# Optimization experiments

Hardware: AMD Instinct MI355X
Metric: run time of the kernel (lower is better)

Reference implementation:

```python
import jax, jax.numpy as jnp
import numpy as np


def _gru(x, h0, Wi, Wh, bi, bh):
    """PyTorch-equations GRU. x: (T,B,D), Wi: (3H,D), Wh: (3H,H). Returns (ys, hT)."""
    xW = jnp.einsum('tbd,gd->tbg', x, Wi) + bi  # (T,B,3H) precomputed input proj
    def step(h, xw):
        hw = h @ Wh.T + bh
        xr, xz, xn = jnp.split(xw, 3, axis=-1)
        hr, hz, hn = jnp.split(hw, 3, axis=-1)
        r = jax.nn.sigmoid(xr + hr)
        z = jax.nn.sigmoid(xz + hz)
        n = jnp.tanh(xn + r * hn)
        h_new = (1.0 - z) * n + z * h
        return h_new, h_new
    hT, ys = jax.lax.scan(step, h0, xW)
    return ys, hT


def _bigru(x, WiF, WhF, biF, bhF, WiB, WhB, biB, bhB):
    B = x.shape[1]
    H = WhF.shape[1]
    h0 = jnp.zeros((B, H), x.dtype)
    yf, hf = _gru(x, h0, WiF, WhF, biF, bhF)
    yb, hb = _gru(x[::-1], h0, WiB, WhB, biB, bhB)
    return jnp.concatenate([yf, yb[::-1]], axis=-1), jnp.stack([hf, hb], axis=0)


def _ln(x, g, b, eps=1e-5):
    mu = x.mean(-1, keepdims=True)
    var = ((x - mu) ** 2).mean(-1, keepdims=True)
    return (x - mu) * jax.lax.rsqrt(var + eps) * g + b


def _forward(tokens, emb,
             s_WiF, s_WhF, s_biF, s_bhF, s_lnF_g, s_lnF_b,
             s_Wi_f, s_Wh_f, s_bi_f, s_bh_f, s_Wi_b, s_Wh_b, s_bi_b, s_bh_b,
             s_ln_g, s_ln_b, s_linW, s_linb,
             d_WiF, d_WhF, d_biF, d_bhF, d_lnF_g, d_lnF_b,
             d_Wi_f, d_Wh_f, d_bi_f, d_bh_f, d_Wi_b, d_Wh_b, d_bi_b, d_bh_b,
             d_ln_g, d_ln_b, out_W, out_b):
    S, T, B = tokens.shape
    H = s_WhF.shape[1]
    # sentence loop is batch-independent -> fold sentences into batch
    x = emb[tokens]                                  # (S,T,B,E)
    x = x.transpose(1, 0, 2, 3).reshape(T, S * B, -1)  # (T, S*B, E)
    h0 = jnp.zeros((S * B, H), x.dtype)
    y, _ = _gru(x, h0, s_WiF, s_WhF, s_biF, s_bhF)
    y = _ln(y, s_lnF_g, s_lnF_b)
    y, _ = _bigru(y, s_Wi_f, s_Wh_f, s_bi_f, s_bh_f, s_Wi_b, s_Wh_b, s_bi_b, s_bh_b)
    y = _ln(y, s_ln_g, s_ln_b)
    y = jnp.tanh(y @ s_linW.T + s_linb)              # (T, S*B, H)
    store = y.mean(axis=0).reshape(S, B, H)          # per-sentence mean-pooled cell
    # document-level encoder over sentence sequence
    h0d = jnp.zeros((B, H), x.dtype)
    y, _ = _gru(store, h0d, d_WiF, d_WhF, d_biF, d_bhF)
    y = _ln(y, d_lnF_g, d_lnF_b)
    y, _ = _bigru(y, d_Wi_f, d_Wh_f, d_bi_f, d_bh_f, d_Wi_b, d_Wh_b, d_bi_b, d_bh_b)
    y = _ln(y, d_ln_g, d_ln_b)
    return jax.nn.sigmoid(y @ out_W.T + out_b)       # (S, B, O)


def setup_inputs() -> dict:
    V, E, H, O = 32000, 256, 256, 2
    S, T, B = 96, 32, 32
    keys = iter(jax.random.split(jax.random.key(0), 64))
    def g(shape, scale=0.06):
        return jax.random.normal(next(keys), shape, jnp.float32) * scale
    inp = {}
    inp['tokens'] = jax.random.randint(next(keys), (S, T, B), 0, V)
    inp['emb'] = g((V, E), 0.1)
    # sentence encoder: uni GRU (E->H), LN(H), bi GRU (H->H), LN(2H), linear 2H->H
    inp['s_WiF'] = g((3 * H, E)); inp['s_WhF'] = g((3 * H, H))
    inp['s_biF'] = jnp.zeros((3 * H,)); inp['s_bhF'] = jnp.zeros((3 * H,))
    inp['s_lnF_g'] = jnp.ones((H,)); inp['s_lnF_b'] = jnp.zeros((H,))
    inp['s_Wi_f'] = g((3 * H, H)); inp['s_Wh_f'] = g((3 * H, H))
    inp['s_bi_f'] = jnp.zeros((3 * H,)); inp['s_bh_f'] = jnp.zeros((3 * H,))
    inp['s_Wi_b'] = g((3 * H, H)); inp['s_Wh_b'] = g((3 * H, H))
    inp['s_bi_b'] = jnp.zeros((3 * H,)); inp['s_bh_b'] = jnp.zeros((3 * H,))
    inp['s_ln_g'] = jnp.ones((2 * H,)); inp['s_ln_b'] = jnp.zeros((2 * H,))
    inp['s_linW'] = g((H, 2 * H)); inp['s_linb'] = jnp.zeros((H,))
    # document encoder: uni GRU (H->H), LN(H), bi GRU (H->H), LN(2H)
    inp['d_WiF'] = g((3 * H, H)); inp['d_WhF'] = g((3 * H, H))
    inp['d_biF'] = jnp.zeros((3 * H,)); inp['d_bhF'] = jnp.zeros((3 * H,))
    inp['d_lnF_g'] = jnp.ones((H,)); inp['d_lnF_b'] = jnp.zeros((H,))
    inp['d_Wi_f'] = g((3 * H, H)); inp['d_Wh_f'] = g((3 * H, H))
    inp['d_bi_f'] = jnp.zeros((3 * H,)); inp['d_bh_f'] = jnp.zeros((3 * H,))
    inp['d_Wi_b'] = g((3 * H, H)); inp['d_Wh_b'] = g((3 * H, H))
    inp['d_bi_b'] = jnp.zeros((3 * H,)); inp['d_bh_b'] = jnp.zeros((3 * H,))
    inp['d_ln_g'] = jnp.ones((2 * H,)); inp['d_ln_b'] = jnp.zeros((2 * H,))
    inp['out_W'] = g((O, 2 * H)); inp['out_b'] = jnp.zeros((O,))
    return inp


def reference(tokens, emb,
              s_WiF, s_WhF, s_biF, s_bhF, s_lnF_g, s_lnF_b,
              s_Wi_f, s_Wh_f, s_bi_f, s_bh_f, s_Wi_b, s_Wh_b, s_bi_b, s_bh_b,
              s_ln_g, s_ln_b, s_linW, s_linb,
              d_WiF, d_WhF, d_biF, d_bhF, d_lnF_g, d_lnF_b,
              d_Wi_f, d_Wh_f, d_bi_f, d_bh_f, d_Wi_b, d_Wh_b, d_bi_b, d_bh_b,
              d_ln_g, d_ln_b, out_W, out_b):
    return _forward(tokens, emb,
                    s_WiF, s_WhF, s_biF, s_bhF, s_lnF_g, s_lnF_b,
                    s_Wi_f, s_Wh_f, s_bi_f, s_bh_f, s_Wi_b, s_Wh_b, s_bi_b, s_bh_b,
                    s_ln_g, s_ln_b, s_linW, s_linb,
                    d_WiF, d_WhF, d_biF, d_bhF, d_lnF_g, d_lnF_b,
                    d_Wi_f, d_Wh_f, d_bi_f, d_bh_f, d_Wi_b, d_Wh_b, d_bi_b, d_bh_b,
                    d_ln_g, d_ln_b, out_W, out_b)
```

## Files before the change

kernel.cpp:

```cpp
#include <hip/hip_runtime.h>


typedef __bf16 bf16;
typedef __bf16 bf16x8 __attribute__((ext_vector_type(8)));
typedef __bf16 bf16x4 __attribute__((ext_vector_type(4)));
typedef float  f32x4  __attribute__((ext_vector_type(4)));

static __device__ __forceinline__ f32x4 mfma16(bf16x8 a, bf16x8 b, f32x4 c) {
  return __builtin_amdgcn_mfma_f32_16x16x32_bf16(a, b, c, 0, 0, 0);
}
static __device__ __forceinline__ float sigm(float x) { return 1.f / (1.f + __expf(-x)); }
static __device__ __forceinline__ bf16x8 asbf(f32x4 v) {
  union { f32x4 f; bf16x8 b; } u; u.f = v; return u.b;
}
static __device__ __forceinline__ void wg_barrier() {
  asm volatile("s_waitcnt lgkmcnt(0)" ::: "memory");
  __builtin_amdgcn_s_barrier();
  __builtin_amdgcn_sched_barrier(0);
}
static __device__ __forceinline__ void gload16(const bf16* g, bf16* l) {
  __builtin_amdgcn_global_load_lds(
      (const __attribute__((address_space(1))) void*)g,
      (__attribute__((address_space(3))) void*)l, 16, 0, 0);
}

__global__ __launch_bounds__(256) void cvt_bf16(
    const float* __restrict__ s, bf16* __restrict__ d, int n4)
{
  int i = blockIdx.x * 256 + threadIdx.x;
  if (i < n4) {
    float4 v = ((const float4*)s)[i];
    bf16x4 o;
    o[0] = (bf16)v.x; o[1] = (bf16)v.y; o[2] = (bf16)v.z; o[3] = (bf16)v.w;
    ((bf16x4*)d)[i] = o;
  }
}

__global__ __launch_bounds__(256) void conv13(
    const float* s0, const float* s1, const float* s2, const float* s3,
    const float* s4, const float* s5, const float* s6, const float* s7,
    const float* s8, const float* s9, const float* s10, const float* s11,
    const float* s12, bf16* __restrict__ dst)
{
  const float* srcs[13] = {s0,s1,s2,s3,s4,s5,s6,s7,s8,s9,s10,s11,s12};
  int m = blockIdx.y;
  int n4 = (m == 12) ? 32768 : 49152;
  int i = blockIdx.x * 256 + threadIdx.x;
  if (i >= n4) return;
  float4 v = ((const float4*)srcs[m])[i];
  bf16x4 o;
  o[0] = (bf16)v.x; o[1] = (bf16)v.y; o[2] = (bf16)v.z; o[3] = (bf16)v.w;
  ((bf16x4*)(dst + (size_t)m * 196608))[i] = o;
}

__global__ __launch_bounds__(256) void prep_bias(
    const float* b0i, const float* b0h, const float* b1i, const float* b1h,
    const float* b2i, const float* b2h, const float* b3i, const float* b3h,
    const float* b4i, const float* b4h, const float* b5i, const float* b5h,
    float* __restrict__ out)
{
  const float* bis[6] = {b0i,b1i,b2i,b3i,b4i,b5i};
  const float* bhs[6] = {b0h,b1h,b2h,b3h,b4h,b5h};
  int g = blockIdx.y;
  int i = blockIdx.x * 256 + threadIdx.x;
  if (i < 768)
    out[g * 768 + i] = bis[g][i] + (i < 512 ? bhs[g][i] : 0.f);
}

__global__ __launch_bounds__(256) void xw_gemm(
    const bf16* __restrict__ X,
    const bf16* __restrict__ W0, const float* __restrict__ b0, bf16* __restrict__ o0,
    const bf16* __restrict__ W1, const float* __restrict__ b1, bf16* __restrict__ o1)
{
  const bf16* W = blockIdx.y ? W1 : W0;
  const float* bias = blockIdx.y ? b1 : b0;
  bf16* out = blockIdx.y ? o1 : o0;
  int wave = (int)blockIdx.x * 4 + (threadIdx.x >> 6);
  int g64 = wave / 48, ct = wave - g64 * 48;
  int lane = threadIdx.x & 63;
  int r16 = lane & 15, g4 = lane >> 4;
  const bf16* wp = W + (size_t)(ct * 16 + r16) * 256;
  const bf16* xb = X + ((size_t)g64 * 64 + r16) * 256;
  f32x4 a0 = {0,0,0,0}, a1 = {0,0,0,0}, a2 = {0,0,0,0}, a3 = {0,0,0,0};
#pragma unroll
  for (int kk = 0; kk < 8; kk++) {
    int k0 = kk * 32 + g4 * 8;
    bf16x8 wf = *(const bf16x8*)(wp + k0);
    a0 = mfma16(*(const bf16x8*)(xb + k0), wf, a0);
    a1 = mfma16(*(const bf16x8*)(xb + 4096 + k0), wf, a1);
    a2 = mfma16(*(const bf16x8*)(xb + 8192 + k0), wf, a2);
    a3 = mfma16(*(const bf16x8*)(xb + 12288 + k0), wf, a3);
  }
  float bv = bias[ct * 16 + r16];
#pragma unroll
  for (int rt = 0; rt < 4; rt++) {
    f32x4 ac = rt == 0 ? a0 : rt == 1 ? a1 : rt == 2 ? a2 : a3;
#pragma unroll
    for (int j = 0; j < 4; j++)
      out[(size_t)(g64 * 64 + rt * 16 + g4 * 4 + j) * 768 + ct * 16 + r16] = (bf16)(ac[j] + bv);
  }
}

__global__ __launch_bounds__(256) void xw_gather_gemm(
    const int* __restrict__ tok, const bf16* __restrict__ embb,
    const bf16* __restrict__ W, const float* __restrict__ bias,
    bf16* __restrict__ out, int c)
{
  int t = blockIdx.y;
  int wave = (int)blockIdx.x * 4 + (threadIdx.x >> 6);
  int g64 = wave / 48, ct = wave - g64 * 48;
  int lane = threadIdx.x & 63;
  int r16 = lane & 15, g4 = lane >> 4;
  const bf16* wp = W + (size_t)(ct * 16 + r16) * 256;
  const bf16* ap[4];
#pragma unroll
  for (int rt = 0; rt < 4; rt++) {
    int n = g64 * 64 + rt * 16 + r16;
    int tk = tok[((n >> 5) << 10) + (t << 5) + (n & 31)];
    ap[rt] = embb + (size_t)tk * 256;
  }
  f32x4 a0 = {0,0,0,0}, a1 = {0,0,0,0}, a2 = {0,0,0,0}, a3 = {0,0,0,0};
#pragma unroll
  for (int kk = 0; kk < 8; kk++) {
    int k0 = kk * 32 + g4 * 8;
    bf16x8 wf = *(const bf16x8*)(wp + k0);
    a0 = mfma16(*(const bf16x8*)(ap[0] + k0), wf, a0);
    a1 = mfma16(*(const bf16x8*)(ap[1] + k0), wf, a1);
    a2 = mfma16(*(const bf16x8*)(ap[2] + k0), wf, a2);
    a3 = mfma16(*(const bf16x8*)(ap[3] + k0), wf, a3);
  }
  float bv = bias[ct * 16 + r16];
#pragma unroll
  for (int rt = 0; rt < 4; rt++) {
    f32x4 ac = rt == 0 ? a0 : rt == 1 ? a1 : rt == 2 ? a2 : a3;
#pragma unroll
    for (int j = 0; j < 4; j++)
      out[((size_t)t * c + g64 * 64 + rt * 16 + g4 * 4 + j) * 768 + ct * 16 + r16] = (bf16)(ac[j] + bv);
  }
}

__global__ __launch_bounds__(1024)
__attribute__((amdgpu_waves_per_eu(4, 4)))
void pgru(
    const bf16* __restrict__ xw0, const bf16* __restrict__ Wh0, const float* __restrict__ bh0,
    const bf16* __restrict__ xw1, const bf16* __restrict__ Wh1, const float* __restrict__ bh1,
    bf16* __restrict__ yout0, bf16* __restrict__ yout1, int ostride,
    const float* __restrict__ lng, const float* __restrict__ lnb,
    int steps, int Mtot, int rev0, int rev1)
{
  int dir = blockIdx.y;
  const bf16*  xw = dir ? xw1 : xw0;
  const bf16*  Wh = dir ? Wh1 : Wh0;
  const float* bh = dir ? bh1 : bh0;
  bf16* yout = dir ? yout1 : yout0;
  int rev = dir ? rev1 : rev0;

  __shared__ __align__(16) bf16 hbuf[16][264];
  __shared__ __align__(16) bf16 xbuf[2][16][3][16][16];

  int tid = threadIdx.x;
  int w = tid >> 6, lane = tid & 63, r16 = lane & 15, g4 = lane >> 4;
  int rowbase = (int)blockIdx.x * 16;
  int c0 = w * 16 + r16;

  for (int i2 = tid; i2 < 528; i2 += 1024) ((bf16x8*)hbuf)[i2] = (bf16x8){};

  f32x4 wr[8], wz[8], wn[8];
  {
    const bf16* W0 = Wh + (size_t)c0 * 256;
#pragma unroll
    for (int kk = 0; kk < 8; kk++) {
      int k0 = kk * 32 + g4 * 8;
      wr[kk] = *(const f32x4*)(W0 + k0);          asm volatile("" : "+v"(wr[kk]));
      wz[kk] = *(const f32x4*)(W0 + 65536 + k0);  asm volatile("" : "+v"(wz[kk]));
      wn[kk] = *(const f32x4*)(W0 + 131072 + k0); asm volatile("" : "+v"(wn[kk]));
    }
  }
  float bhn0 = bh[c0 + 512];

  int m_ = (lane & 31) >> 1;
  int k_ = (lane & 1) * 8;
  int gsel = (lane >> 5) * 256;
  auto stage = [&](int b, int st) {
    const bf16* s1 = xw + ((size_t)st * Mtot + rowbase + m_) * 768 + gsel + w * 16 + k_;
    gload16(s1,       &xbuf[b][w][0][0][0]);
    gload16(s1 + 256, &xbuf[b][w][1][0][0]);
  };
  stage(0, rev ? steps - 1 : 0);

  for (int i = 0; i < steps; i++) {
    int cur = i & 1;
    int st = rev ? steps - 1 - i : i;
    if (i + 1 < steps) {
      stage(cur ^ 1, rev ? steps - 2 - i : i + 1);
      asm volatile("s_waitcnt vmcnt(2)" ::: "memory");
    } else {
      asm volatile("s_waitcnt vmcnt(0)" ::: "memory");
    }
    __builtin_amdgcn_sched_barrier(0);
    wg_barrier();

    f32x4 a0 = {0,0,0,0}, a1 = {0,0,0,0}, a2 = {0,0,0,0};
#pragma unroll
    for (int kk = 0; kk < 8; kk++) {
      bf16x8 a = *(const bf16x8*)&hbuf[r16][kk * 32 + g4 * 8];
      a0 = mfma16(a, asbf(wr[kk]), a0);
      a1 = mfma16(a, asbf(wz[kk]), a1);
      a2 = mfma16(a, asbf(wn[kk]), a2);
    }
    float hn[4];
#pragma unroll
    for (int j = 0; j < 4; j++) {
      int m = g4 * 4 + j;
      float r = sigm((float)xbuf[cur][w][0][m][r16] + a0[j]);
      float z = sigm((float)xbuf[cur][w][1][m][r16] + a1[j]);
      float n = tanhf((float)xbuf[cur][w][2][m][r16] + r * (a2[j] + bhn0));
      hn[j] = (1.f - z) * n + z * (float)hbuf[m][c0];
    }
    wg_barrier();
#pragma unroll
    for (int j = 0; j < 4; j++)
      hbuf[g4 * 4 + j][c0] = (bf16)hn[j];
    if (!lng) {
#pragma unroll
      for (int j = 0; j < 4; j++) {
        size_t ro = ((size_t)st * Mtot + rowbase + g4 * 4 + j) * ostride;
        yout[ro + c0] = (bf16)hn[j];
      }
    } else {
      wg_barrier();
      bf16x4 v4 = *(const bf16x4*)&hbuf[w][lane * 4];
      float v[4]; float sm = 0.f, sq = 0.f;
#pragma unroll
      for (int j = 0; j < 4; j++) { v[j] = (float)v4[j]; sm += v[j]; sq += v[j] * v[j]; }
      for (int msk = 32; msk; msk >>= 1) { sm += __shfl_xor(sm, msk); sq += __shfl_xor(sq, msk); }
      float mu  = sm * (1.f / 256.f);
      float var = sq * (1.f / 256.f) - mu * mu;
      float inv = rsqrtf(fmaxf(var, 0.f) + 1e-5f);
      bf16x4 o;
#pragma unroll
      for (int j = 0; j < 4; j++)
        o[j] = (bf16)((v[j] - mu) * inv * lng[lane * 4 + j] + lnb[lane * 4 + j]);
      *(bf16x4*)&yout[((size_t)st * Mtot + rowbase + w) * ostride + lane * 4] = o;
    }
  }
}

__global__ __launch_bounds__(256) void sent_tail_part(
    const bf16* __restrict__ hf, const bf16* __restrict__ hb,
    const float* __restrict__ gam, const float* __restrict__ bet,
    const bf16* __restrict__ W, const float* __restrict__ bias,
    float* __restrict__ part, int c)
{
  int wave = threadIdx.x >> 6;
  int lane = threadIdx.x & 63;
  int r16 = lane & 15, g4 = lane >> 4;
  int r0 = (int)blockIdx.x << 4;
  int tg = blockIdx.y;
  size_t rowoff = (size_t)(r0 + r16) * 256;

  f32x4 ms0 = {0,0,0,0}, ms1 = {0,0,0,0}, ms2 = {0,0,0,0}, ms3 = {0,0,0,0};

  for (int tt = 0; tt < 4; tt++) {
    int t = tg * 4 + tt;
    const bf16* pf = hf + (size_t)t * c * 256 + rowoff;
    const bf16* pb = hb + (size_t)t * c * 256 + rowoff;
    bf16x8 xv[16];
    float s = 0.f, sq = 0.f;
#pragma unroll
    for (int kk = 0; kk < 16; kk++) {
      int k0 = kk * 32 + g4 * 8;
      xv[kk] = (kk < 8) ? *(const bf16x8*)(pf + k0) : *(const bf16x8*)(pb + k0 - 256);
#pragma unroll
      for (int j = 0; j < 8; j++) { float f = (float)xv[kk][j]; s += f; sq += f * f; }
    }
    s  += __shfl_xor(s, 16);  s  += __shfl_xor(s, 32);
    sq += __shfl_xor(sq, 16); sq += __shfl_xor(sq, 32);
    float mu  = s * (1.f / 512.f);
    float var = sq * (1.f / 512.f) - mu * mu;
    float inv = rsqrtf(fmaxf(var, 0.f) + 1e-5f);
#pragma unroll
    for (int kk = 0; kk < 16; kk++) {
      int k0 = kk * 32 + g4 * 8;
      float ga[8], be[8];
      *(float4*)(ga)     = *(const float4*)(gam + k0);
      *(float4*)(ga + 4) = *(const float4*)(gam + k0 + 4);
      *(float4*)(be)     = *(const float4*)(bet + k0);
      *(float4*)(be + 4) = *(const float4*)(bet + k0 + 4);
#pragma unroll
      for (int j = 0; j < 8; j++)
        xv[kk][j] = (bf16)(((float)xv[kk][j] - mu) * inv * ga[j] + be[j]);
    }
#pragma unroll
    for (int tc = 0; tc < 4; tc++) {
      int cj = wave * 64 + tc * 16;
      const bf16* wp = W + (size_t)(cj + r16) * 512;
      f32x4 acc = {0,0,0,0};
#pragma unroll
      for (int kk = 0; kk < 16; kk++)
        acc = mfma16(xv[kk], *(const bf16x8*)(wp + kk * 32 + g4 * 8), acc);
      float bb = bias[cj + r16];
      f32x4* msp = (tc == 0) ? &ms0 : (tc == 1) ? &ms1 : (tc == 2) ? &ms2 : &ms3;
#pragma unroll
      for (int j = 0; j < 4; j++) (*msp)[j] += tanhf(acc[j] + bb);
    }
  }
#pragma unroll
  for (int tc = 0; tc < 4; tc++) {
    int cj = wave * 64 + tc * 16;
    f32x4 ms = (tc == 0) ? ms0 : (tc == 1) ? ms1 : (tc == 2) ? ms2 : ms3;
#pragma unroll
    for (int j = 0; j < 4; j++)
      part[((size_t)tg * c + r0 + g4 * 4 + j) * 256 + cj + r16] = ms[j];
  }
}

__global__ __launch_bounds__(256) void tail_reduce(
    const float* __restrict__ part, bf16* __restrict__ out, int c)
{
  int idx = blockIdx.x * 256 + threadIdx.x;
  float s = 0.f;
#pragma unroll
  for (int g = 0; g < 8; g++) s += part[(size_t)g * c * 256 + idx];
  out[idx] = (bf16)(s * 0.03125f);
}

__global__ __launch_bounds__(256) void ln_out_head(
    const bf16* __restrict__ X, const float* __restrict__ lng, const float* __restrict__ lnb,
    const float* __restrict__ W, const float* __restrict__ bias, float* __restrict__ out)
{
  int w = threadIdx.x >> 6, lane = threadIdx.x & 63;
  int row = (int)blockIdx.x * 4 + w;
  bf16x8 v8 = *(const bf16x8*)&X[(size_t)row * 512 + lane * 8];
  float v[8]; float sm = 0.f, sq = 0.f;
#pragma unroll
  for (int j = 0; j < 8; j++) { v[j] = (float)v8[j]; sm += v[j]; sq += v[j] * v[j]; }
  for (int msk = 32; msk; msk >>= 1) { sm += __shfl_xor(sm, msk); sq += __shfl_xor(sq, msk); }
  float mu  = sm * (1.f / 512.f);
  float var = sq * (1.f / 512.f) - mu * mu;
  float inv = rsqrtf(fmaxf(var, 0.f) + 1e-5f);
  float a0 = 0.f, a1 = 0.f;
  int base = lane * 8;
#pragma unroll
  for (int j = 0; j < 8; j++) {
    float y = (v[j] - mu) * inv * lng[base + j] + lnb[base + j];
    a0 += y * W[base + j];
    a1 += y * W[512 + base + j];
  }
  for (int msk = 32; msk; msk >>= 1) { a0 += __shfl_xor(a0, msk); a1 += __shfl_xor(a1, msk); }
  if (lane == 0) {
    out[(size_t)row * 2 + 0] = sigm(a0 + bias[0]);
    out[(size_t)row * 2 + 1] = sigm(a1 + bias[1]);
  }
}

extern "C" void kernel_launch(void* const* d_in, const int* in_sizes, int n_in,
                              void* d_out, int out_size, void* d_ws, size_t ws_size,
                              hipStream_t stream)
{
  (void)in_sizes; (void)n_in; (void)out_size;
  const int*   tokens = (const int*)d_in[0];
  const float* emb    = (const float*)d_in[1];
  auto fp = [&](int i) { return (const float*)d_in[i]; };
  const float *s_WiF = fp(2),  *s_WhF = fp(3),  *s_biF = fp(4),  *s_bhF = fp(5);
  const float *s_lnF_g = fp(6), *s_lnF_b = fp(7);
  const float *s_Wi_f = fp(8),  *s_Wh_f = fp(9),  *s_bi_f = fp(10), *s_bh_f = fp(11);
  const float *s_Wi_b = fp(12), *s_Wh_b = fp(13), *s_bi_b = fp(14), *s_bh_b = fp(15);
  const float *s_ln_g = fp(16), *s_ln_b = fp(17), *s_linW = fp(18), *s_linb = fp(19);
  const float *dWiF = fp(20), *dWhF = fp(21), *dbiF = fp(22), *dbhF = fp(23);
  const float *d_lnF_g = fp(24), *d_lnF_b = fp(25);
  const float *dWi_f = fp(26), *dWh_f = fp(27), *dbi_f = fp(28), *dbh_f = fp(29);
  const float *dWi_b = fp(30), *dWh_b = fp(31), *dbi_b = fp(32), *dbh_b = fp(33);
  const float *d_ln_g = fp(34), *d_ln_b = fp(35), *out_W = fp(36), *out_b = fp(37);

  const int T = 32, S = 96;
  const int GW = 196608;

  bf16* wc = (bf16*)d_ws;
  bf16 *c_sWiF = wc,         *c_sWhF = wc + GW;
  bf16 *c_sWif = wc + 2*GW,  *c_sWhf = wc + 3*GW;
  bf16 *c_sWib = wc + 4*GW,  *c_sWhb = wc + 5*GW;
  bf16 *c_dWiF = wc + 6*GW,  *c_dWhF = wc + 7*GW;
  bf16 *c_dWif = wc + 8*GW,  *c_dWhf = wc + 9*GW;
  bf16 *c_dWib = wc + 10*GW, *c_dWhb = wc + 11*GW;
  bf16 *c_linW = wc + 12*GW;
  const size_t WB = (size_t)(12 * GW + 131072) * 2;
  bf16* embb = (bf16*)((char*)d_ws + WB);
  const size_t EB = (size_t)32000 * 256 * 2;
  float* bmod = (float*)((char*)d_ws + WB + EB);
  const size_t BMB = 6 * 768 * 4;

  conv13<<<dim3(192, 13), 256, 0, stream>>>(
      s_WiF, s_WhF, s_Wi_f, s_Wh_f, s_Wi_b, s_Wh_b,
      dWiF, dWhF, dWi_f, dWh_f, dWi_b, dWh_b, s_linW, wc);
  cvt_bf16<<<8000, 256, 0, stream>>>(emb, embb, 2048000);
  prep_bias<<<dim3(3, 6), 256, 0, stream>>>(
      s_biF, s_bhF, s_bi_f, s_bh_f, s_bi_b, s_bh_b,
      dbiF, dbhF, dbi_f, dbh_f, dbi_b, dbh_b, bmod);
  const float *bm_sF = bmod, *bm_sf = bmod + 768, *bm_sb = bmod + 1536;
  const float *bm_dF = bmod + 2304, *bm_df = bmod + 3072, *bm_db = bmod + 3840;

  char* ws = (char*)d_ws + WB + EB + BMB;
  bf16* store = (bf16*)ws;
  bf16* yd1ln = store + (size_t)3072 * 256;
  bf16* ybid  = yd1ln + (size_t)3072 * 256;
  bf16* xw_u  = ybid  + (size_t)3072 * 512;
  bf16* xwdf  = xw_u  + (size_t)3072 * 768;
  bf16* xwdb  = xwdf  + (size_t)3072 * 768;
  const size_t fixedB = WB + EB + BMB
      + ((size_t)3072 * 256 * 2 + (size_t)3072 * 512 + (size_t)3 * 3072 * 768) * 2;

  int c = 3072;
  while (c > 192 && fixedB + (size_t)98304 * c > ws_size) c >>= 1;
  char* cb = (char*)d_ws + fixedB;
  bf16*  xw   = (bf16*)cb;
  bf16*  y1ln = (bf16*)(cb + (size_t)49152 * c);
  bf16*  hf   = (bf16*)(cb + (size_t)65536 * c);
  bf16*  hb   = (bf16*)(cb + (size_t)81920 * c);
  float* part = (float*)cb;

  for (int base = 0; base < 3072; base += c) {
    const int* tkb = tokens + (size_t)base * 32;
    xw_gather_gemm<<<dim3((c / 64) * 12, T), 256, 0, stream>>>(
        tkb, embb, c_sWiF, bm_sF, xw, c);
    pgru<<<dim3(c / 16, 1), 1024, 0, stream>>>(
        xw, c_sWhF, s_bhF, nullptr, nullptr, nullptr,
        y1ln, nullptr, 256, s_lnF_g, s_lnF_b, T, c, 0, 0);
    xw_gemm<<<dim3((T * c / 64) * 12, 1), 256, 0, stream>>>(
        y1ln, c_sWif, bm_sf, xw, nullptr, nullptr, nullptr);
    pgru<<<dim3(c / 16, 1), 1024, 0, stream>>>(
        xw, c_sWhf, s_bh_f, nullptr, nullptr, nullptr,
        hf, nullptr, 256, nullptr, nullptr, T, c, 0, 0);
    xw_gemm<<<dim3((T * c / 64) * 12, 1), 256, 0, stream>>>(
        y1ln, c_sWib, bm_sb, xw, nullptr, nullptr, nullptr);
    pgru<<<dim3(c / 16, 1), 1024, 0, stream>>>(
        xw, c_sWhb, s_bh_b, nullptr, nullptr, nullptr,
        hb, nullptr, 256, nullptr, nullptr, T, c, 1, 0);
    sent_tail_part<<<dim3(c / 16, 8), 256, 0, stream>>>(
        hf, hb, s_ln_g, s_ln_b, c_linW, s_linb, part, c);
    tail_reduce<<<c, 256, 0, stream>>>(part, store + (size_t)base * 256, c);
  }

  xw_gemm<<<dim3((3072 / 64) * 12, 1), 256, 0, stream>>>(
      store, c_dWiF, bm_dF, xw_u, nullptr, nullptr, nullptr);
  pgru<<<dim3(2, 1), 1024, 0, stream>>>(
      xw_u, c_dWhF, dbhF, nullptr, nullptr, nullptr,
      yd1ln, nullptr, 256, d_lnF_g, d_lnF_b, S, 32, 0, 0);
  xw_gemm<<<dim3((3072 / 64) * 12, 2), 256, 0, stream>>>(
      yd1ln, c_dWif, bm_df, xwdf, c_dWib, bm_db, xwdb);
  pgru<<<dim3(2, 2), 1024, 0, stream>>>(
      xwdf, c_dWhf, dbh_f, xwdb, c_dWhb, dbh_b,
      ybid, ybid + 256, 512, nullptr, nullptr, S, 32, 0, 1);
  ln_out_head<<<768, 256, 0, stream>>>(ybid, d_ln_g, d_ln_b, out_W, out_b,
                                       (float*)d_out);
}
```

Before: 3.632 ms.

## Double rows per GRU block and stream recurrent weights from memory each step

The recurrent GRU kernel now uses 512-thread blocks that each handle 32 batch rows, with every wave computing a 2x2 grid of 16x16 tiles. Recurrent weights are reloaded from global memory every step instead of being pinned in registers, which removes the register-residency constraint and halves block count. The input-projection staging is widened to cover all three gates for 32 rows. This trades extra per-step global/L2 traffic and longer serial latency per step for more MFMA work per hidden-state read.

After: 7.842 ms. 116% more time.

```diff
diff --git a/kernel.cpp b/kernel.cpp
--- a/kernel.cpp
+++ b/kernel.cpp
@@ -10,9 +10,6 @@
   return __builtin_amdgcn_mfma_f32_16x16x32_bf16(a, b, c, 0, 0, 0);
 }
 static __device__ __forceinline__ float sigm(float x) { return 1.f / (1.f + __expf(-x)); }
-static __device__ __forceinline__ bf16x8 asbf(f32x4 v) {
-  union { f32x4 f; bf16x8 b; } u; u.f = v; return u.b;
-}
 static __device__ __forceinline__ void wg_barrier() {
   asm volatile("s_waitcnt lgkmcnt(0)" ::: "memory");
   __builtin_amdgcn_s_barrier();
@@ -139,8 +136,7 @@
   }
 }
 
-__global__ __launch_bounds__(1024)
-__attribute__((amdgpu_waves_per_eu(4, 4)))
+__global__ __launch_bounds__(512)
 void pgru(
     const bf16* __restrict__ xw0, const bf16* __restrict__ Wh0, const float* __restrict__ bh0,
     const bf16* __restrict__ xw1, const bf16* __restrict__ Wh1, const float* __restrict__ bh1,
@@ -155,93 +151,129 @@
   bf16* yout = dir ? yout1 : yout0;
   int rev = dir ? rev1 : rev0;
 
-  __shared__ __align__(16) bf16 hbuf[16][264];
-  __shared__ __align__(16) bf16 xbuf[2][16][3][16][16];
+  __shared__ __align__(16) bf16 hbuf[32][280];
+  __shared__ __align__(16) bf16 xbuf[2][8][3][32][32];
 
   int tid = threadIdx.x;
   int w = tid >> 6, lane = tid & 63, r16 = lane & 15, g4 = lane >> 4;
-  int rowbase = (int)blockIdx.x * 16;
-  int c0 = w * 16 + r16;
-
-  for (int i2 = tid; i2 < 528; i2 += 1024) ((bf16x8*)hbuf)[i2] = (bf16x8){};
-
-  f32x4 wr[8], wz[8], wn[8];
-  {
-    const bf16* W0 = Wh + (size_t)c0 * 256;
-#pragma unroll
-    for (int kk = 0; kk < 8; kk++) {
-      int k0 = kk * 32 + g4 * 8;
-      wr[kk] = *(const f32x4*)(W0 + k0);          asm volatile("" : "+v"(wr[kk]));
-      wz[kk] = *(const f32x4*)(W0 + 65536 + k0);  asm volatile("" : "+v"(wz[kk]));
-      wn[kk] = *(const f32x4*)(W0 + 131072 + k0); asm volatile("" : "+v"(wn[kk]));
-    }
-  }
-  float bhn0 = bh[c0 + 512];
-
-  int m_ = (lane & 31) >> 1;
-  int k_ = (lane & 1) * 8;
-  int gsel = (lane >> 5) * 256;
+  int rowbase = (int)blockIdx.x * 32;
+  int c0 = w * 32 + r16, c1 = c0 + 16;
+
+  for (int i2 = tid; i2 < 1120; i2 += 512) ((bf16x8*)hbuf)[i2] = (bf16x8){};
+
+  float bhn0 = bh[c0 + 512], bhn1 = bh[c1 + 512];
+
+  int rr_ = lane >> 2;
+  int kc_ = (lane & 3) * 8;
   auto stage = [&](int b, int st) {
-    const bf16* s1 = xw + ((size_t)st * Mtot + rowbase + m_) * 768 + gsel + w * 16 + k_;
-    gload16(s1,       &xbuf[b][w][0][0][0]);
-    gload16(s1 + 256, &xbuf[b][w][1][0][0]);
+    const bf16* base = xw + ((size_t)st * Mtot + rowbase) * 768 + w * 32 + kc_;
+#pragma unroll
+    for (int g = 0; g < 3; g++) {
+      gload16(base + (size_t)rr_ * 768 + g * 256,        &xbuf[b][w][g][0][0]);
+      gload16(base + (size_t)(16 + rr_) * 768 + g * 256, &xbuf[b][w][g][16][0]);
+    }
   };
   stage(0, rev ? steps - 1 : 0);
+  wg_barrier();
 
   for (int i = 0; i < steps; i++) {
     int cur = i & 1;
     int st = rev ? steps - 1 - i : i;
     if (i + 1 < steps) {
       stage(cur ^ 1, rev ? steps - 2 - i : i + 1);
-      asm volatile("s_waitcnt vmcnt(2)" ::: "memory");
+      asm volatile("s_waitcnt vmcnt(6)" ::: "memory");
     } else {
       asm volatile("s_waitcnt vmcnt(0)" ::: "memory");
     }
     __builtin_amdgcn_sched_barrier(0);
+
+    const bf16* wp0 = Wh + (size_t)c0 * 256;
+    const bf16* wp1 = Wh + (size_t)c1 * 256;
+    asm volatile("" : "+v"(wp0), "+v"(wp1));
+
+    f32x4 aR00={0,0,0,0}, aR01={0,0,0,0}, aR10={0,0,0,0}, aR11={0,0,0,0};
+    f32x4 aZ00={0,0,0,0}, aZ01={0,0,0,0}, aZ10={0,0,0,0}, aZ11={0,0,0,0};
+    f32x4 aN00={0,0,0,0}, aN01={0,0,0,0}, aN10={0,0,0,0}, aN11={0,0,0,0};
+#pragma unroll
+    for (int kk = 0; kk < 8; kk++) {
+      int ko = kk * 32 + g4 * 8;
+      bf16x8 wr0 = *(const bf16x8*)(wp0 + ko);
+      bf16x8 wz0 = *(const bf16x8*)(wp0 + 65536 + ko);
+      bf16x8 wn0 = *(const bf16x8*)(wp0 + 131072 + ko);
+      bf16x8 wr1 = *(const bf16x8*)(wp1 + ko);
+      bf16x8 wz1 = *(const bf16x8*)(wp1 + 65536 + ko);
+      bf16x8 wn1 = *(const bf16x8*)(wp1 + 131072 + ko);
+      bf16x8 a0 = *(const bf16x8*)&hbuf[r16][ko];
+      bf16x8 a1 = *(const bf16x8*)&hbuf[16 + r16][ko];
+      aR00 = mfma16(a0, wr0, aR00); aR01 = mfma16(a1, wr0, aR01);
+      aZ00 = mfma16(a0, wz0, aZ00); aZ01 = mfma16(a1, wz0, aZ01);
+      aN00 = mfma16(a0, wn0, aN00); aN01 = mfma16(a1, wn0, aN01);
+      aR10 = mfma16(a0, wr1, aR10); aR11 = mfma16(a1, wr1, aR11);
+      aZ10 = mfma16(a0, wz1, aZ10); aZ11 = mfma16(a1, wz1, aZ11);
+      aN10 = mfma16(a0, wn1, aN10); aN11 = mfma16(a1, wn1, aN11);
+    }
+
+    float hn00[4], hn01[4], hn10[4], hn11[4];
+#pragma unroll
+    for (int j = 0; j < 4; j++) {
+      int m0 = g4 * 4 + j, m1 = 16 + m0;
+      { float r = sigm((float)xbuf[cur][w][0][m0][r16] + aR00[j]);
+        float z = sigm((float)xbuf[cur][w][1][m0][r16] + aZ00[j]);
+        float n = tanhf((float)xbuf[cur][w][2][m0][r16] + r * (aN00[j] + bhn0));
+        hn00[j] = (1.f - z) * n + z * (float)hbuf[m0][c0]; }
+      { float r = sigm((float)xbuf[cur][w][0][m1][r16] + aR01[j]);
+        float z = sigm((float)xbuf[cur][w][1][m1][r16] + aZ01[j]);
+        float n = tanhf((float)xbuf[cur][w][2][m1][r16] + r * (aN01[j] + bhn0));
+        hn01[j] = (1.f - z) * n + z * (float)hbuf[m1][c0]; }
+      { float r = sigm((float)xbuf[cur][w][0][m0][16 + r16] + aR10[j]);
+        float z = sigm((float)xbuf[cur][w][1][m0][16 + r16] + aZ10[j]);
+        float n = tanhf((float)xbuf[cur][w][2][m0][16 + r16] + r * (aN10[j] + bhn1));
+        hn10[j] = (1.f - z) * n + z * (float)hbuf[m0][c1]; }
+      { float r = sigm((float)xbuf[cur][w][0][m1][16 + r16] + aR11[j]);
+        float z = sigm((float)xbuf[cur][w][1][m1][16 + r16] + aZ11[j]);
+        float n = tanhf((float)xbuf[cur][w][2][m1][16 + r16] + r * (aN11[j] + bhn1));
+        hn11[j] = (1.f - z) * n + z * (float)hbuf[m1][c1]; }
+    }
     wg_barrier();
-
-    f32x4 a0 = {0,0,0,0}, a1 = {0,0,0,0}, a2 = {0,0,0,0};
-#pragma unroll
-    for (int kk = 0; kk < 8; kk++) {
-      bf16x8 a = *(const bf16x8*)&hbuf[r16][kk * 32 + g4 * 8];
-      a0 = mfma16(a, asbf(wr[kk]), a0);
-      a1 = mfma16(a, asbf(wz[kk]), a1);
-      a2 = mfma16(a, asbf(wn[kk]), a2);
-    }
-    float hn[4];
 #pragma unroll
     for (int j = 0; j < 4; j++) {
-      int m = g4 * 4 + j;
-      float r = sigm((float)xbuf[cur][w][0][m][r16] + a0[j]);
-      float z = sigm((float)xbuf[cur][w][1][m][r16] + a1[j]);
-      float n = tanhf((float)xbuf[cur][w][2][m][r16] + r * (a2[j] + bhn0));
-      hn[j] = (1.f - z) * n + z * (float)hbuf[m][c0];
+      int m0 = g4 * 4 + j, m1 = 16 + m0;
+      hbuf[m0][c0] = (bf16)hn00[j];
+      hbuf[m1][c0] = (bf16)hn01[j];
+      hbuf[m0][c1] = (bf16)hn10[j];
+      hbuf[m1][c1] = (bf16)hn11[j];
+    }
+    if (!lng) {
+#pragma unroll
+      for (int j = 0; j < 4; j++) {
+        int m0 = g4 * 4 + j, m1 = 16 + m0;
+        size_t r0 = ((size_t)st * Mtot + rowbase + m0) * ostride;
+        size_t r1 = ((size_t)st * Mtot + rowbase + m1) * ostride;
+        yout[r0 + c0] = (bf16)hn00[j];
+        yout[r1 + c0] = (bf16)hn01[j];
+        yout[r0 + c1] = (bf16)hn10[j];
+        yout[r1 + c1] = (bf16)hn11[j];
+      }
     }
     wg_barrier();
-#pragma unroll
-    for (int j = 0; j < 4; j++)
-      hbuf[g4 * 4 + j][c0] = (bf16)hn[j];
-    if (!lng) {
-#pragma unroll
-      for (int j = 0; j < 4; j++) {
-        size_t ro = ((size_t)st * Mtot + rowbase + g4 * 4 + j) * ostride;
-        yout[ro + c0] = (bf16)hn[j];
+    if (lng) {
+#pragma unroll
+      for (int rr = 0; rr < 4; rr++) {
+        int r = w * 4 + rr;
+        bf16x4 v4 = *(const bf16x4*)&hbuf[r][lane * 4];
+        float v[4]; float sm = 0.f, sq = 0.f;
+#pragma unroll
+        for (int j = 0; j < 4; j++) { v[j] = (float)v4[j]; sm += v[j]; sq += v[j] * v[j]; }
+        for (int msk = 32; msk; msk >>= 1) { sm += __shfl_xor(sm, msk); sq += __shfl_xor(sq, msk); }
+        float mu  = sm * (1.f / 256.f);
+        float var = sq * (1.f / 256.f) - mu * mu;
+        float inv = rsqrtf(fmaxf(var, 0.f) + 1e-5f);
+        bf16x4 o;
+#pragma unroll
+        for (int j = 0; j < 4; j++)
+          o[j] = (bf16)((v[j] - mu) * inv * lng[lane * 4 + j] + lnb[lane * 4 + j]);
+        *(bf16x4*)&yout[((size_t)st * Mtot + rowbase + r) * ostride + lane * 4] = o;
       }
-    } else {
-      wg_barrier();
-      bf16x4 v4 = *(const bf16x4*)&hbuf[w][lane * 4];
-      float v[4]; float sm = 0.f, sq = 0.f;
-#pragma unroll
-      for (int j = 0; j < 4; j++) { v[j] = (float)v4[j]; sm += v[j]; sq += v[j] * v[j]; }
-      for (int msk = 32; msk; msk >>= 1) { sm += __shfl_xor(sm, msk); sq += __shfl_xor(sq, msk); }
-      float mu  = sm * (1.f / 256.f);
-      float var = sq * (1.f / 256.f) - mu * mu;
-      float inv = rsqrtf(fmaxf(var, 0.f) + 1e-5f);
-      bf16x4 o;
-#pragma unroll
-      for (int j = 0; j < 4; j++)
-        o[j] = (bf16)((v[j] - mu) * inv * lng[lane * 4 + j] + lnb[lane * 4 + j]);
-      *(bf16x4*)&yout[((size_t)st * Mtot + rowbase + w) * ostride + lane * 4] = o;
     }
   }
 }
@@ -423,17 +455,17 @@
     const int* tkb = tokens + (size_t)base * 32;
     xw_gather_gemm<<<dim3((c / 64) * 12, T), 256, 0, stream>>>(
         tkb, embb, c_sWiF, bm_sF, xw, c);
-    pgru<<<dim3(c / 16, 1), 1024, 0, stream>>>(
+    pgru<<<dim3(c / 32, 1), 512, 0, stream>>>(
         xw, c_sWhF, s_bhF, nullptr, nullptr, nullptr,
         y1ln, nullptr, 256, s_lnF_g, s_lnF_b, T, c, 0, 0);
     xw_gemm<<<dim3((T * c / 64) * 12, 1), 256, 0, stream>>>(
         y1ln, c_sWif, bm_sf, xw, nullptr, nullptr, nullptr);
-    pgru<<<dim3(c / 16, 1), 1024, 0, stream>>>(
+    pgru<<<dim3(c / 32, 1), 512, 0, stream>>>(
         xw, c_sWhf, s_bh_f, nullptr, nullptr, nullptr,
         hf, nullptr, 256, nullptr, nullptr, T, c, 0, 0);
     xw_gemm<<<dim3((T * c / 64) * 12, 1), 256, 0, stream>>>(
         y1ln, c_sWib, bm_sb, xw, nullptr, nullptr, nullptr);
-    pgru<<<dim3(c / 16, 1), 1024, 0, stream>>>(
+    pgru<<<dim3(c / 32, 1), 512, 0, stream>>>(
         xw, c_sWhb, s_bh_b, nullptr, nullptr, nullptr,
         hb, nullptr, 256, nullptr, nullptr, T, c, 1, 0);
     sent_tail_part<<<dim3(c / 16, 8), 256, 0, stream>>>(
@@ -443,12 +475,12 @@
 
   xw_gemm<<<dim3((3072 / 64) * 12, 1), 256, 0, stream>>>(
       store, c_dWiF, bm_dF, xw_u, nullptr, nullptr, nullptr);
-  pgru<<<dim3(2, 1), 1024, 0, stream>>>(
+  pgru<<<dim3(1, 1), 512, 0, stream>>>(
       xw_u, c_dWhF, dbhF, nullptr, nullptr, nullptr,
       yd1ln, nullptr, 256, d_lnF_g, d_lnF_b, S, 32, 0, 0);
   xw_gemm<<<dim3((3072 / 64) * 12, 2), 256, 0, stream>>>(
       yd1ln, c_dWif, bm_df, xwdf, c_dWib, bm_db, xwdb);
-  pgru<<<dim3(2, 2), 1024, 0, stream>>>(
+  pgru<<<dim3(1, 2), 512, 0, stream>>>(
       xwdf, c_dWhf, dbh_f, xwdb, c_dWhb, dbh_b,
       ybid, ybid + 256, 512, nullptr, nullptr, S, 32, 0, 1);
   ln_out_head<<<768, 256, 0, stream>>>(ybid, d_ln_g, d_ln_b, out_W, out_b,
```
